# Performance work log

Hardware: AMD Instinct MI355X
Metric: run time of the kernel (lower is better)

The kernel has to match this reference:

```python
import jax, jax.numpy as jnp
import numpy as np

DK = 64
DROPOUT_P = 0.1


def setup_inputs() -> dict:
    key = jax.random.key(0)
    kq, kk, kv, km = jax.random.split(key, 4)
    B, S, D = 16, 2048, 64
    q = jax.random.normal(kq, (B, S, D), dtype=jnp.float32)
    k = jax.random.normal(kk, (B, S, D), dtype=jnp.float32)
    v = jax.random.normal(kv, (B, S, D), dtype=jnp.float32)
    attn_mask = jax.random.randint(km, (S, S), 0, 2, dtype=jnp.int32)
    return {"q": q, "k": k, "v": v, "attn_mask": attn_mask}


def reference(q, k, v, attn_mask):
    # q = q / sqrt(dk)
    qs = q * (1.0 / np.sqrt(DK)).astype(np.float32)
    # dots: [B, S_q, S_k]
    dots = jnp.einsum("bqd,bkd->bqk", qs, k)
    # mask: 0 -> -inf, 1 -> 0 (additive)
    add_mask = jnp.where(attn_mask == 0, -jnp.inf, 0.0).astype(dots.dtype)
    dots = dots + add_mask  # broadcast [S,S] over batch
    attn = jax.nn.softmax(dots, axis=-1)
    # inverted dropout, train mode, fixed key for determinism
    keep = jax.random.bernoulli(jax.random.key(42), 1.0 - DROPOUT_P, attn.shape)
    attn = jnp.where(keep, attn * (1.0 / (1.0 - DROPOUT_P)), 0.0)
    out = jnp.einsum("bqk,bkd->bqd", attn, v)
    return out
```

## Files before the change

kernel.cpp:

```cpp
#include <hip/hip_runtime.h>

#define BATCH 16
#define SEQ   2048
#define DIM   64
#define NTHREADS 256
#define NROWS    (BATCH * SEQ)
#define OUTELEMS (NROWS * DIM)

typedef short bf16x8 __attribute__((ext_vector_type(8)));
typedef float f32x4 __attribute__((ext_vector_type(4)));

__device__ __forceinline__ int ldsoff(int row) {
  return row * 72 + 16 * (row >> 2);
}
#define LDS_SZ (64 * 72 + 16 * 16)

__device__ __forceinline__ unsigned tf_bits(unsigned f) {
  unsigned x0 = 0u;
  unsigned x1 = f;
  const unsigned ks1 = 42u;
  const unsigned ks2 = 0x1BD11BDAu ^ 42u;
  x1 += ks1;
#define TF_R(r) { x0 += x1; x1 = __builtin_amdgcn_alignbit(x1, x1, 32u - (r)); x1 ^= x0; }
  TF_R(13) TF_R(15) TF_R(26) TF_R(6)
  x0 += ks1; x1 += ks2 + 1u;
  TF_R(17) TF_R(29) TF_R(16) TF_R(24)
  x0 += ks2; x1 += 2u;
  TF_R(13) TF_R(15) TF_R(26) TF_R(6)
  x1 += ks1 + 3u;
  TF_R(17) TF_R(29) TF_R(16) TF_R(24)
  x0 += ks1; x1 += ks2 + 4u;
  TF_R(13) TF_R(15) TF_R(26) TF_R(6)
  x0 += ks2; x1 += 5u;
#undef TF_R
  return x0 ^ x1;
}
#define KEEP_THRESH 0xE6666600u

__device__ __forceinline__ unsigned pack_bf16x2(float lo, float hi) {
  const unsigned l = (__float_as_uint(lo) + 0x8000u) >> 16;
  const unsigned h = (__float_as_uint(hi) + 0x8000u) & 0xFFFF0000u;
  return h | l;
}
__device__ __forceinline__ unsigned pack_trunc(float lo, float hi) {
  return __builtin_amdgcn_perm(__float_as_uint(hi), __float_as_uint(lo), 0x07060302u);
}

#define WS_KF 0
#define WS_VF 1048576

__global__ __launch_bounds__(NTHREADS)
void convert_kv(const float* __restrict__ k, const float* __restrict__ v,
                unsigned* __restrict__ ws) {
  const unsigned gid = blockIdx.x * NTHREADS + threadIdx.x;
  const unsigned e = gid & 262143u;
  const int lane = e & 63;
  const int ks = (e >> 6) & 1, nt = (e >> 7) & 3, kt = (e >> 9) & 31, b = e >> 14;
  const int tx = lane & 15, quad = lane >> 4;
  uint4 wout;
  if (gid < 262144u) {
    const float* src = k + ((size_t)b * SEQ + kt * 64 + 4 * tx + nt) * DIM
                         + ks * 32 + quad * 8;
    const float4 f0 = *(const float4*)src;
    const float4 f1 = *(const float4*)(src + 4);
    wout.x = pack_bf16x2(f0.x, f0.y); wout.y = pack_bf16x2(f0.z, f0.w);
    wout.z = pack_bf16x2(f1.x, f1.y); wout.w = pack_bf16x2(f1.z, f1.w);
    *(uint4*)(ws + WS_KF + (size_t)e * 4) = wout;
  } else {
    const float* src = v + ((size_t)b * SEQ + kt * 64 + ks * 32 + quad * 8) * DIM
                         + nt * 16 + tx;
    const float a0 = src[0 * DIM], a1 = src[1 * DIM], a2 = src[2 * DIM], a3 = src[3 * DIM];
    const float a4 = src[4 * DIM], a5 = src[5 * DIM], a6 = src[6 * DIM], a7 = src[7 * DIM];
    wout.x = pack_bf16x2(a0, a1); wout.y = pack_bf16x2(a2, a3);
    wout.z = pack_bf16x2(a4, a5); wout.w = pack_bf16x2(a6, a7);
    *(uint4*)(ws + WS_VF + (size_t)e * 4) = wout;
  }
}

__global__ __launch_bounds__(NTHREADS, 2)
void attn_fwd(const float* __restrict__ q, const unsigned* __restrict__ ws,
              const int* __restrict__ mask, float* __restrict__ out) {
  __shared__ unsigned short PS[LDS_SZ];

  const int t    = threadIdx.x;
  const int w    = t >> 6;
  const int lane = t & 63;
  const int tx   = lane & 15;
  const int quad = lane >> 4;

  const int bb = blockIdx.x >> 5;
  const int q0 = (blockIdx.x & 31) * 64;
  const int qw = q0 + 16 * w;

  const float qscale = 0.125f * 1.44269504088896340736f;

  bf16x8 aq[2];
  {
    const float* qr = q + ((size_t)bb * SEQ + qw + tx) * DIM + quad * 8;
#pragma unroll
    for (int ks = 0; ks < 2; ++ks) {
      const float4 f0 = *(const float4*)(qr + ks * 32);
      const float4 f1 = *(const float4*)(qr + ks * 32 + 4);
      union { unsigned u[4]; bf16x8 v; } a;
      a.u[0] = pack_bf16x2(f0.x * qscale, f0.y * qscale);
      a.u[1] = pack_bf16x2(f0.z * qscale, f0.w * qscale);
      a.u[2] = pack_bf16x2(f1.x * qscale, f1.y * qscale);
      a.u[3] = pack_bf16x2(f1.z * qscale, f1.w * qscale);
      aq[ks] = a.v;
    }
  }

  float lrun[4] = {0.f, 0.f, 0.f, 0.f};
  f32x4 oacc[4];
#pragma unroll
  for (int nt = 0; nt < 4; ++nt) oacc[nt] = (f32x4){0.f, 0.f, 0.f, 0.f};

  const unsigned* kfb = ws + WS_KF + (size_t)(bb * 32) * 2048 + (size_t)lane * 4;
  const unsigned* vfb = ws + WS_VF + (size_t)(bb * 32) * 2048 + (size_t)lane * 4;
  const int* mbase = mask + (size_t)(qw + quad * 4) * SEQ + 4 * tx;
  const unsigned fbase0 = (unsigned)(bb * SEQ + qw + quad * 4) * (unsigned)SEQ
                          + (unsigned)(4 * tx);

  bf16x8 vfA[4][2], vfB[4][2];

#define RNG_PWRITE(kt_, qk_)                                                   \
  {                                                                            \
    const unsigned fb = fbase0 + (unsigned)((kt_) * 64);                       \
    _Pragma("unroll")                                                          \
    for (int reg = 0; reg < 4; ++reg) {                                        \
      const int* mreg = (const int*)&mv[reg];                                  \
      float pd[4];                                                             \
      float ls = 0.0f;                                                         \
      _Pragma("unroll")                                                        \
      for (int nt = 0; nt < 4; ++nt) {                                         \
        const float s = mreg[nt] ? qk_[nt][reg] : -1e30f;                      \
        const float e = __builtin_amdgcn_exp2f(s);                             \
        ls += e;                                                               \
        const unsigned bits = tf_bits(fb + (unsigned)(reg * SEQ) + (unsigned)nt); \
        pd[nt] = (bits < KEEP_THRESH) ? e : 0.0f;                              \
      }                                                                        \
      lrun[reg] += ls;                                                         \
      uint2 pw;                                                                \
      pw.x = pack_trunc(pd[0], pd[1]);                                         \
      pw.y = pack_trunc(pd[2], pd[3]);                                         \
      *(uint2*)&PS[ldsoff(16 * w + quad * 4 + reg) + 4 * tx] = pw;             \
    }                                                                          \
  }

  {
    const unsigned* kfp = kfb;
    const unsigned* vfp = vfb;
    bf16x8 kf[4][2];
#pragma unroll
    for (int nt = 0; nt < 4; ++nt)
#pragma unroll
      for (int ks = 0; ks < 2; ++ks) {
        kf[nt][ks]  = *(const bf16x8*)(kfp + (nt * 2 + ks) * 256);
        vfA[nt][ks] = *(const bf16x8*)(vfp + (nt * 2 + ks) * 256);
      }
    int4 mv[4];
#pragma unroll
    for (int reg = 0; reg < 4; ++reg)
      mv[reg] = *(const int4*)(mbase + (size_t)reg * SEQ);
    f32x4 qk[4];
#pragma unroll
    for (int nt = 0; nt < 4; ++nt) {
      f32x4 c = (f32x4){0.f, 0.f, 0.f, 0.f};
#pragma unroll
      for (int ks = 0; ks < 2; ++ks)
        c = __builtin_amdgcn_mfma_f32_16x16x32_bf16(aq[ks], kf[nt][ks], c, 0, 0, 0);
      qk[nt] = c;
    }
    RNG_PWRITE(0, qk)
  }

#define BODY(kt_, prevV, curV)                                                 \
  {                                                                            \
    const unsigned* kfp = kfb + (size_t)(kt_) * 2048;                          \
    const unsigned* vfp = vfb + (size_t)(kt_) * 2048;                          \
    bf16x8 kf[4][2];                                                           \
    _Pragma("unroll")                                                          \
    for (int nt = 0; nt < 4; ++nt)                                             \
      _Pragma("unroll")                                                        \
      for (int ks = 0; ks < 2; ++ks) {                                         \
        kf[nt][ks]   = *(const bf16x8*)(kfp + (nt * 2 + ks) * 256);            \
        curV[nt][ks] = *(const bf16x8*)(vfp + (nt * 2 + ks) * 256);            \
      }                                                                        \
    int4 mv[4];                                                                \
    _Pragma("unroll")                                                          \
    for (int reg = 0; reg < 4; ++reg)                                          \
      mv[reg] = *(const int4*)(mbase + (size_t)reg * SEQ + (kt_) * 64);        \
    _Pragma("unroll")                                                          \
    for (int ks = 0; ks < 2; ++ks) {                                           \
      const bf16x8 ap = *(const bf16x8*)&PS[ldsoff(16 * w + tx) + ks * 32 + quad * 8]; \
      _Pragma("unroll")                                                        \
      for (int nt = 0; nt < 4; ++nt)                                           \
        oacc[nt] = __builtin_amdgcn_mfma_f32_16x16x32_bf16(ap, prevV[nt][ks],  \
                                                           oacc[nt], 0, 0, 0); \
    }                                                                          \
    f32x4 qk[4];                                                               \
    _Pragma("unroll")                                                          \
    for (int nt = 0; nt < 4; ++nt) {                                           \
      f32x4 c = (f32x4){0.f, 0.f, 0.f, 0.f};                                   \
      _Pragma("unroll")                                                        \
      for (int ks = 0; ks < 2; ++ks)                                           \
        c = __builtin_amdgcn_mfma_f32_16x16x32_bf16(aq[ks], kf[nt][ks], c, 0, 0, 0); \
      qk[nt] = c;                                                              \
    }                                                                          \
    RNG_PWRITE(kt_, qk)                                                        \
  }

#pragma unroll 1
  for (int kt = 1; kt < 31; kt += 2) {
    BODY(kt, vfA, vfB)
    BODY(kt + 1, vfB, vfA)
  }
  BODY(31, vfA, vfB)

#pragma unroll
  for (int ks = 0; ks < 2; ++ks) {
    const bf16x8 ap = *(const bf16x8*)&PS[ldsoff(16 * w + tx) + ks * 32 + quad * 8];
#pragma unroll
    for (int nt = 0; nt < 4; ++nt)
      oacc[nt] = __builtin_amdgcn_mfma_f32_16x16x32_bf16(ap, vfB[nt][ks], oacc[nt], 0, 0, 0);
  }

  float linv[4];
#pragma unroll
  for (int reg = 0; reg < 4; ++reg) {
    float ls = lrun[reg];
    ls += __shfl_xor(ls, 1);
    ls += __shfl_xor(ls, 2);
    ls += __shfl_xor(ls, 4);
    ls += __shfl_xor(ls, 8);
    linv[reg] = (1.0f / 0.9f) / ls;
  }
  float* ob = out + ((size_t)bb * SEQ + qw) * DIM;
#pragma unroll
  for (int nt = 0; nt < 4; ++nt)
#pragma unroll
    for (int reg = 0; reg < 4; ++reg)
      ob[(size_t)(quad * 4 + reg) * DIM + nt * 16 + tx] = oacc[nt][reg] * linv[reg];
}

extern "C" void kernel_launch(void* const* d_in, const int* in_sizes, int n_in,
                              void* d_out, int out_size, void* d_ws, size_t ws_size,
                              hipStream_t stream) {
  const float* q = (const float*)d_in[0];
  const float* k = (const float*)d_in[1];
  const float* v = (const float*)d_in[2];
  const int* mask = (const int*)d_in[3];
  float* out = (float*)d_out;
  unsigned* ws = (unsigned*)d_ws;

  hipLaunchKernelGGL(convert_kv, dim3(2048), dim3(NTHREADS), 0, stream, k, v, ws);
  hipLaunchKernelGGL(attn_fwd, dim3(512), dim3(NTHREADS), 0, stream,
                     q, ws, mask, out);
}
```

Before: 231.1 us.

## Split KV range across two blocks with atomic accumulation and combine pass

Splits each query tile's key sequence into two halves handled by separate blocks (1024 blocks instead of 512). Partial outputs and row sums are accumulated with float atomics into zeroed buffers, and a separate combine kernel normalizes afterward. Launch bounds are raised to 4 blocks per SM. The aim is better occupancy and wave-count balance on the GPU's many CUs, at the cost of two memsets, atomic traffic, an extra kernel pass, and register pressure from the tighter launch bounds.

```diff
diff --git a/kernel.cpp b/kernel.cpp
--- a/kernel.cpp
+++ b/kernel.cpp
@@ -48,6 +48,8 @@
 
 #define WS_KF 0
 #define WS_VF 1048576
+#define WS_L  2097152
+#define WS_NEED ((size_t)(WS_L + NROWS) * 4)
 
 __global__ __launch_bounds__(NTHREADS)
 void convert_kv(const float* __restrict__ k, const float* __restrict__ v,
@@ -77,9 +79,11 @@
   }
 }
 
-__global__ __launch_bounds__(NTHREADS, 2)
+template <int SPLIT>
+__global__ __launch_bounds__(NTHREADS, 4)
 void attn_fwd(const float* __restrict__ q, const unsigned* __restrict__ ws,
-              const int* __restrict__ mask, float* __restrict__ out) {
+              const int* __restrict__ mask, float* __restrict__ out,
+              float* __restrict__ lsum) {
   __shared__ unsigned short PS[LDS_SZ];
 
   const int t    = threadIdx.x;
@@ -88,9 +92,14 @@
   const int tx   = lane & 15;
   const int quad = lane >> 4;
 
-  const int bb = blockIdx.x >> 5;
-  const int q0 = (blockIdx.x & 31) * 64;
+  int bid = blockIdx.x;
+  const int half = SPLIT ? (bid >> 9) : 0;
+  bid &= 511;
+  const int bb = bid >> 5;
+  const int q0 = (bid & 31) * 64;
   const int qw = q0 + 16 * w;
+  const int kt0 = SPLIT ? half * 16 : 0;
+  const int NT  = SPLIT ? 16 : 32;
 
   const float qscale = 0.125f * 1.44269504088896340736f;
 
@@ -115,17 +124,17 @@
 #pragma unroll
   for (int nt = 0; nt < 4; ++nt) oacc[nt] = (f32x4){0.f, 0.f, 0.f, 0.f};
 
-  const unsigned* kfb = ws + WS_KF + (size_t)(bb * 32) * 2048 + (size_t)lane * 4;
-  const unsigned* vfb = ws + WS_VF + (size_t)(bb * 32) * 2048 + (size_t)lane * 4;
-  const int* mbase = mask + (size_t)(qw + quad * 4) * SEQ + 4 * tx;
+  const unsigned* kfb = ws + WS_KF + (size_t)(bb * 32 + kt0) * 2048 + (size_t)lane * 4;
+  const unsigned* vfb = ws + WS_VF + (size_t)(bb * 32 + kt0) * 2048 + (size_t)lane * 4;
+  const int* mbase = mask + (size_t)(qw + quad * 4) * SEQ + 4 * tx + kt0 * 64;
   const unsigned fbase0 = (unsigned)(bb * SEQ + qw + quad * 4) * (unsigned)SEQ
-                          + (unsigned)(4 * tx);
+                          + (unsigned)(4 * tx) + (unsigned)(kt0 * 64);
 
   bf16x8 vfA[4][2], vfB[4][2];
 
-#define RNG_PWRITE(kt_, qk_)                                                   \
+#define RNG_PWRITE(jt_, qk_)                                                   \
   {                                                                            \
-    const unsigned fb = fbase0 + (unsigned)((kt_) * 64);                       \
+    const unsigned fb = fbase0 + (unsigned)((jt_) * 64);                       \
     _Pragma("unroll")                                                          \
     for (int reg = 0; reg < 4; ++reg) {                                        \
       const int* mreg = (const int*)&mv[reg];                                  \
@@ -148,15 +157,13 @@
   }
 
   {
-    const unsigned* kfp = kfb;
-    const unsigned* vfp = vfb;
     bf16x8 kf[4][2];
 #pragma unroll
     for (int nt = 0; nt < 4; ++nt)
 #pragma unroll
       for (int ks = 0; ks < 2; ++ks) {
-        kf[nt][ks]  = *(const bf16x8*)(kfp + (nt * 2 + ks) * 256);
-        vfA[nt][ks] = *(const bf16x8*)(vfp + (nt * 2 + ks) * 256);
+        kf[nt][ks]  = *(const bf16x8*)(kfb + (nt * 2 + ks) * 256);
+        vfA[nt][ks] = *(const bf16x8*)(vfb + (nt * 2 + ks) * 256);
       }
     int4 mv[4];
 #pragma unroll
@@ -174,10 +181,10 @@
     RNG_PWRITE(0, qk)
   }
 
-#define BODY(kt_, prevV, curV)                                                 \
+#define BODY(jt_, prevV, curV)                                                 \
   {                                                                            \
-    const unsigned* kfp = kfb + (size_t)(kt_) * 2048;                          \
-    const unsigned* vfp = vfb + (size_t)(kt_) * 2048;                          \
+    const unsigned* kfp = kfb + (size_t)(jt_) * 2048;                          \
+    const unsigned* vfp = vfb + (size_t)(jt_) * 2048;                          \
     bf16x8 kf[4][2];                                                           \
     _Pragma("unroll")                                                          \
     for (int nt = 0; nt < 4; ++nt)                                             \
@@ -189,7 +196,7 @@
     int4 mv[4];                                                                \
     _Pragma("unroll")                                                          \
     for (int reg = 0; reg < 4; ++reg)                                          \
-      mv[reg] = *(const int4*)(mbase + (size_t)reg * SEQ + (kt_) * 64);        \
+      mv[reg] = *(const int4*)(mbase + (size_t)reg * SEQ + (jt_) * 64);        \
     _Pragma("unroll")                                                          \
     for (int ks = 0; ks < 2; ++ks) {                                           \
       const bf16x8 ap = *(const bf16x8*)&PS[ldsoff(16 * w + tx) + ks * 32 + quad * 8]; \
@@ -207,15 +214,15 @@
         c = __builtin_amdgcn_mfma_f32_16x16x32_bf16(aq[ks], kf[nt][ks], c, 0, 0, 0); \
       qk[nt] = c;                                                              \
     }                                                                          \
-    RNG_PWRITE(kt_, qk)                                                        \
+    RNG_PWRITE(jt_, qk)                                                        \
   }
 
 #pragma unroll 1
-  for (int kt = 1; kt < 31; kt += 2) {
-    BODY(kt, vfA, vfB)
-    BODY(kt + 1, vfB, vfA)
-  }
-  BODY(31, vfA, vfB)
+  for (int jt = 1; jt < NT - 1; jt += 2) {
+    BODY(jt, vfA, vfB)
+    BODY(jt + 1, vfB, vfA)
+  }
+  BODY(NT - 1, vfA, vfB)
 
 #pragma unroll
   for (int ks = 0; ks < 2; ++ks) {
@@ -225,7 +232,7 @@
       oacc[nt] = __builtin_amdgcn_mfma_f32_16x16x32_bf16(ap, vfB[nt][ks], oacc[nt], 0, 0, 0);
   }
 
-  float linv[4];
+  float lred[4];
 #pragma unroll
   for (int reg = 0; reg < 4; ++reg) {
     float ls = lrun[reg];
@@ -233,14 +240,35 @@
     ls += __shfl_xor(ls, 2);
     ls += __shfl_xor(ls, 4);
     ls += __shfl_xor(ls, 8);
-    linv[reg] = (1.0f / 0.9f) / ls;
+    lred[reg] = ls;
   }
   float* ob = out + ((size_t)bb * SEQ + qw) * DIM;
-#pragma unroll
-  for (int nt = 0; nt < 4; ++nt)
-#pragma unroll
-    for (int reg = 0; reg < 4; ++reg)
-      ob[(size_t)(quad * 4 + reg) * DIM + nt * 16 + tx] = oacc[nt][reg] * linv[reg];
+  if (SPLIT) {
+    if (tx == 0) {
+#pragma unroll
+      for (int reg = 0; reg < 4; ++reg)
+        atomicAdd(&lsum[bb * SEQ + qw + quad * 4 + reg], lred[reg]);
+    }
+#pragma unroll
+    for (int nt = 0; nt < 4; ++nt)
+#pragma unroll
+      for (int reg = 0; reg < 4; ++reg)
+        atomicAdd(&ob[(size_t)(quad * 4 + reg) * DIM + nt * 16 + tx], oacc[nt][reg]);
+  } else {
+#pragma unroll
+    for (int nt = 0; nt < 4; ++nt)
+#pragma unroll
+      for (int reg = 0; reg < 4; ++reg)
+        ob[(size_t)(quad * 4 + reg) * DIM + nt * 16 + tx] =
+            oacc[nt][reg] * ((1.0f / 0.9f) / lred[reg]);
+  }
+}
+
+__global__ __launch_bounds__(NTHREADS)
+void combine(float* __restrict__ out, const float* __restrict__ lsum) {
+  const int gid = blockIdx.x * NTHREADS + threadIdx.x;
+  const int row = gid >> 6;
+  out[gid] = out[gid] * (1.0f / (0.9f * lsum[row]));
 }
 
 extern "C" void kernel_launch(void* const* d_in, const int* in_sizes, int n_in,
@@ -254,6 +282,15 @@
   unsigned* ws = (unsigned*)d_ws;
 
   hipLaunchKernelGGL(convert_kv, dim3(2048), dim3(NTHREADS), 0, stream, k, v, ws);
-  hipLaunchKernelGGL(attn_fwd, dim3(512), dim3(NTHREADS), 0, stream,
-                     q, ws, mask, out);
-}
+  if (ws_size >= WS_NEED) {
+    hipMemsetAsync(out, 0, (size_t)out_size * 4, stream);
+    hipMemsetAsync((float*)d_ws + WS_L, 0, (size_t)NROWS * 4, stream);
+    hipLaunchKernelGGL(attn_fwd<1>, dim3(1024), dim3(NTHREADS), 0, stream,
+                       q, ws, mask, out, (float*)d_ws + WS_L);
+    hipLaunchKernelGGL(combine, dim3(OUTELEMS / NTHREADS), dim3(NTHREADS), 0, stream,
+                       out, (const float*)d_ws + WS_L);
+  } else {
+    hipLaunchKernelGGL(attn_fwd<0>, dim3(512), dim3(NTHREADS), 0, stream,
+                       q, ws, mask, out, (float*)d_ws + WS_L);
+  }
+}
```

Measured after the change: 233.7 us. No clear change (+1.1%).
